# Optimization experiments

Measured on AMD Instinct MI355X. Metric: run time of the kernel, lower is better.

Reference implementation:

```python
import jax, jax.numpy as jnp
import numpy as np

K = 5            # kernel_size per dim
KD = K ** 3      # 125 spline weight slots
DIM = 3
NUM_GRAPHS = 64
# (n_nodes, n_edges, c_in, c_mid, c_out) per pyramid level
LEVELS = [(20000, 320000, 1, 32, 64), (10000, 160000, 1, 64, 64),
          (5000, 80000, 1, 64, 64), (2500, 40000, 1, 64, 64), (1250, 20000, 1, 64, 64)]


def setup_inputs() -> dict:
    key = jax.random.key(0)
    inp = {}
    for i, (n, e, cin, c1, c2) in enumerate(LEVELS, start=1):
        ks = jax.random.split(jax.random.fold_in(key, i), 8)
        inp[f'x{i}'] = jax.random.normal(ks[0], (n, cin), jnp.float32)
        inp[f'pseudo{i}'] = jax.random.uniform(ks[1], (e, DIM), jnp.float32)  # in [0,1)
        inp[f'edge_index{i}'] = jax.random.randint(ks[2], (2, e), 0, n)
        inp[f'batch{i}'] = jnp.sort(jax.random.randint(ks[3], (n,), 0, NUM_GRAPHS))
        inp[f'W{i}a'] = 0.1 * jax.random.normal(ks[4], (KD, cin, c1), jnp.float32)
        inp[f'root{i}a'] = 0.1 * jax.random.normal(ks[5], (cin, c1), jnp.float32)
        inp[f'bias{i}a'] = jnp.zeros((c1,), jnp.float32)
        inp[f'W{i}b'] = 0.1 * jax.random.normal(ks[6], (KD, c1, c2), jnp.float32)
        inp[f'root{i}b'] = 0.1 * jax.random.normal(ks[7], (c1, c2), jnp.float32)
        inp[f'bias{i}b'] = jnp.zeros((c2,), jnp.float32)
    kf = jax.random.fold_in(key, 99)
    inp['fc_w'] = 0.05 * jax.random.normal(kf, (5 * 64, 10), jnp.float32)
    inp['fc_b'] = jnp.zeros((10,), jnp.float32)
    return inp


def _spline_conv(x, src, dst, pseudo, W, Wroot, bias):
    """Degree-1 open B-spline conv (torch_spline_conv), mean aggregation + root weight."""
    n, cin = x.shape
    v = pseudo * (K - 1)                       # [E,3], pseudo in [0,1)
    k0 = jnp.floor(v).astype(jnp.int32)        # lower knot index per dim
    frac = v - k0                              # fractional part per dim
    xs = x[src]                                # [E,cin] gather source feats
    # accumulate basis-weighted source features per (target node, kernel slot)
    acc = jnp.zeros((n, KD, cin), x.dtype)
    for bits in range(2 ** DIM):               # 8 corner combinations of linear spline
        w = jnp.ones((src.shape[0],), x.dtype)
        idx = jnp.zeros((src.shape[0],), jnp.int32)
        for d in range(DIM):
            b = (bits >> d) & 1
            w = w * (frac[:, d] if b else 1.0 - frac[:, d])
            idx = idx * K + (k0[:, d] + b)
        acc = acc.at[dst, idx].add(w[:, None] * xs)
    deg = jnp.zeros((n,), x.dtype).at[dst].add(1.0)
    out = jnp.einsum('nki,kio->no', acc, W) / jnp.maximum(deg, 1.0)[:, None]
    return out + x @ Wroot + bias


def _readout(f, batch):
    s = jax.ops.segment_sum(f, batch, num_segments=NUM_GRAPHS)
    cnt = jax.ops.segment_sum(jnp.ones((f.shape[0],), f.dtype), batch, num_segments=NUM_GRAPHS)
    return s / jnp.maximum(cnt, 1.0)[:, None]   # scatter_mean


def _level(x, ei, ps, bt, Wa, ra, ba, Wb, rb, bb):
    f = jax.nn.relu(_spline_conv(x, ei[0], ei[1], ps, Wa, ra, ba))
    f = jax.nn.relu(_spline_conv(f, ei[0], ei[1], ps, Wb, rb, bb))
    return _readout(f, bt)


def reference(x1, pseudo1, edge_index1, batch1, W1a, root1a, bias1a, W1b, root1b, bias1b,
              x2, pseudo2, edge_index2, batch2, W2a, root2a, bias2a, W2b, root2b, bias2b,
              x3, pseudo3, edge_index3, batch3, W3a, root3a, bias3a, W3b, root3b, bias3b,
              x4, pseudo4, edge_index4, batch4, W4a, root4a, bias4a, W4b, root4b, bias4b,
              x5, pseudo5, edge_index5, batch5, W5a, root5a, bias5a, W5b, root5b, bias5b,
              fc_w, fc_b):
    levels = [
        (x1, edge_index1, pseudo1, batch1, W1a, root1a, bias1a, W1b, root1b, bias1b),
        (x2, edge_index2, pseudo2, batch2, W2a, root2a, bias2a, W2b, root2b, bias2b),
        (x3, edge_index3, pseudo3, batch3, W3a, root3a, bias3a, W3b, root3b, bias3b),
        (x4, edge_index4, pseudo4, batch4, W4a, root4a, bias4a, W4b, root4b, bias4b),
        (x5, edge_index5, pseudo5, batch5, W5a, root5a, bias5a, W5b, root5b, bias5b),
    ]
    res = [_level(*lv) for lv in levels]
    h = jnp.concatenate(res, axis=1)            # [B,320]; eval mode -> dropout is identity
    logits = h @ fc_w + fc_b                    # [B,10]
    return jax.nn.log_softmax(logits, axis=1)
```

## Files before the change

### kernel.cpp

```cpp
#include <hip/hip_runtime.h>
#include <hip/hip_fp16.h>
#include <math.h>

#define NUM_GRAPHS 64

typedef unsigned short ushortT;
typedef __attribute__((ext_vector_type(8))) short bf16x8;
typedef __attribute__((ext_vector_type(4))) float f32x4;

constexpr int cN[5]       = {20000, 10000, 5000, 2500, 1250};
constexpr int cE[5]       = {320000, 160000, 80000, 40000, 20000};
constexpr int cNOFF[6]    = {0, 20000, 30000, 35000, 37500, 38750};
constexpr int cEOFF[6]    = {0, 320000, 480000, 560000, 600000, 620000};
constexpr int cEBLKOFF[6] = {0, 1250, 1875, 2188, 2345, 2424};
constexpr int cNBLKOFF[6] = {0, 79, 119, 139, 149, 154};
constexpr int cMT[5]      = {5064, 2564, 1314, 689, 377};
constexpr int cTILEOFF[6] = {0, 5064, 7628, 8942, 9631, 10008};
constexpr int cSEOFF[6]   = {0, 324096, 488192, 572288, 616384, 640512};
constexpr int cF1OFF[6]   = {0, 640000, 1280000, 1600000, 1760000, 1840000};
constexpr int cWOFF[6]    = {0, 32000, 96000, 160000, 224000, 288000};
constexpr int cABLK[6]    = {0, 1250, 1875, 2188, 2345, 2424};
constexpr int cRBOFF[5]   = {0, 256, 768, 1280, 1792};
constexpr int cWAOFF[6]   = {0, 512, 1536, 2560, 3584, 4608};
constexpr int cRGB[6]     = {0, 313, 470, 549, 589, 609};
constexpr int cPAIR[6]    = {0, 2532, 3814, 4471, 4816, 5005};

struct P5f { const float* p[5]; };
struct P5i { const int* p[5]; };

__device__ __forceinline__ int lvl_e(int b) {
    return (b >= cEBLKOFF[4]) ? 4 : (b >= cEBLKOFF[3]) ? 3 : (b >= cEBLKOFF[2]) ? 2 : (b >= cEBLKOFF[1]) ? 1 : 0;
}
__device__ __forceinline__ int lvl_n(int b) {
    return (b >= cNBLKOFF[4]) ? 4 : (b >= cNBLKOFF[3]) ? 3 : (b >= cNBLKOFF[2]) ? 2 : (b >= cNBLKOFF[1]) ? 1 : 0;
}

__device__ __forceinline__ ushortT f2bf(float f) {
    union { float f; unsigned int u; } v; v.f = f;
    unsigned int r = (v.u + 0x7FFFu + ((v.u >> 16) & 1u)) >> 16;
    return (ushortT)r;
}
__device__ __forceinline__ float h2f_lo(unsigned int u) {
    return __half2float(__ushort_as_half((ushortT)(u & 0xFFFFu)));
}
__device__ __forceinline__ float h2f_hi(unsigned int u) {
    return __half2float(__ushort_as_half((ushortT)(u >> 16)));
}

__global__ void k_hist(P5f PS, P5i EI, int* __restrict__ dcnt, int* __restrict__ bb) {
    int b = blockIdx.x;
    int l = lvl_e(b);
    int lb = b - cEBLKOFF[l];
    int E = cE[l];
    __shared__ int h[64];
    int t = threadIdx.x;
    if (t < 64) h[t] = 0;
    __syncthreads();
    int e = lb * 256 + t;
    if (e < E) {
        atomicAdd(&dcnt[cNOFF[l] + EI.p[l][E + e]], 1);
        const float* ps = PS.p[l];
        int c = (int)floorf(ps[e * 3] * 4.f) * 16 + (int)floorf(ps[e * 3 + 1] * 4.f) * 4
              + (int)floorf(ps[e * 3 + 2] * 4.f);
        atomicAdd(&h[c], 1);
    }
    __syncthreads();
    if (t < 64) bb[(size_t)b * 64 + t] = h[t];
}

__global__ void k_cellscan(int* __restrict__ bb_all, int* __restrict__ csPad,
                           int* __restrict__ cellTot, int* __restrict__ cot_all) {
    int l = blockIdx.x;
    int c = threadIdx.x;
    int* bb = bb_all + (size_t)cEBLKOFF[l] * 64;
    int nblk = cEBLKOFF[l + 1] - cEBLKOFF[l];
    int run = 0;
    int b = 0;
    for (; b + 16 <= nblk; b += 16) {
        int v[16];
#pragma unroll
        for (int u = 0; u < 16; u++) v[u] = bb[(b + u) * 64 + c];
#pragma unroll
        for (int u = 0; u < 16; u++) { bb[(b + u) * 64 + c] = run; run += v[u]; }
    }
    for (; b < nblk; b++) { int v = bb[b * 64 + c]; bb[b * 64 + c] = run; run += v; }
    int tot = run;
    cellTot[l * 64 + c] = tot;
    int tiles = (tot + 63) >> 6;
    int x = tiles;
#pragma unroll
    for (int off = 1; off < 64; off <<= 1) { int y = __shfl_up(x, off, 64); if (c >= off) x += y; }
    int tileBase = x - tiles;
    csPad[l * 64 + c] = tileBase * 64;
    int* cot = cot_all + cTILEOFF[l];
    for (int i = 0; i < tiles; i++) {
        int vv = tot - (i << 6); if (vv > 64) vv = 64;
        cot[tileBase + i] = c | (vv << 8);
    }
    int nT = __shfl(x, 63, 64);
    int mt = cMT[l];
    for (int i = nT + c; i < mt; i += 64) cot[i] = -1;
}

__global__ void k_nscan1(const int* __restrict__ dcnt, int* __restrict__ dbase, int* __restrict__ bsum) {
    int b = blockIdx.x;
    int l = lvl_n(b);
    int lb = b - cNBLKOFF[l];
    int n = cN[l];
    __shared__ int sh[256];
    int t = threadIdx.x;
    int i = lb * 256 + t;
    int v = (i < n) ? dcnt[cNOFF[l] + i] : 0;
    sh[t] = v;
    __syncthreads();
    for (int off = 1; off < 256; off <<= 1) {
        int y = (t >= off) ? sh[t - off] : 0;
        __syncthreads();
        sh[t] += y;
        __syncthreads();
    }
    if (i < n) dbase[cNOFF[l] + i] = sh[t] - v;
    if (t == 255) bsum[b] = sh[255];
}

__global__ void k_nscan2(const int* __restrict__ bsum, int* __restrict__ boff) {
    int l = blockIdx.x;
    int o = cNBLKOFF[l];
    int nb = cNBLKOFF[l + 1] - o;
    int t = threadIdx.x;
    int v = (t < nb) ? bsum[o + t] : 0;
    int s = v;
#pragma unroll
    for (int off = 1; off < 64; off <<= 1) { int y = __shfl_up(s, off, 64); if (t >= off) s += y; }
    int tot = __shfl(s, 63, 64);
    if (t < nb) boff[o + t] = s - v;
    int t2 = t + 64;
    int v2 = (t2 < nb) ? bsum[o + t2] : 0;
    int s2 = v2;
#pragma unroll
    for (int off = 1; off < 64; off <<= 1) { int y = __shfl_up(s2, off, 64); if (t >= off) s2 += y; }
    if (t2 < nb) boff[o + t2] = tot + s2 - v2;
}

__global__ void k_scatter(P5f PS, P5i EI, const int* __restrict__ bb, const int* __restrict__ csPad,
                          const int* __restrict__ dbase, const int* __restrict__ boff,
                          int* __restrict__ rank,
                          int4* __restrict__ cbrec, int4* __restrict__ darec,
                          int* __restrict__ cpos) {
    int b = blockIdx.x;
    int l = lvl_e(b);
    int lb = b - cEBLKOFF[l];
    int E = cE[l];
    __shared__ int base[64];
    __shared__ int cnt[64];
    int t = threadIdx.x;
    if (t < 64) { base[t] = bb[(size_t)b * 64 + t] + csPad[l * 64 + t]; cnt[t] = 0; }
    __syncthreads();
    int e = lb * 256 + t;
    if (e >= E) return;
    const float* ps = PS.p[l];
    float v0 = ps[e * 3] * 4.f, v1 = ps[e * 3 + 1] * 4.f, v2 = ps[e * 3 + 2] * 4.f;
    float f0 = floorf(v0), f1v = floorf(v1), f2v = floorf(v2);
    int c = (int)f0 * 16 + (int)f1v * 4 + (int)f2v;
    int r = atomicAdd(&cnt[c], 1);
    int posc = base[c] + r;
    const int* ei = EI.p[l];
    int src = ei[e];
    int dst = ei[E + e];
    int posd = dbase[cNOFF[l] + dst] + boff[cNBLKOFF[l] + (dst >> 8)]
             + atomicAdd(&rank[cNOFF[l] + dst], 1);
    unsigned int fxfy = (unsigned int)__half_as_ushort(__float2half(v0 - f0))
                      | ((unsigned int)__half_as_ushort(__float2half(v1 - f1v)) << 16);
    unsigned int fzp  = (unsigned int)__half_as_ushort(__float2half(v2 - f2v));
    int4 rc;
    rc.x = src; rc.y = 0; rc.z = (int)fxfy; rc.w = (int)fzp;
    cbrec[cSEOFF[l] + posc] = rc;
    int4 rd;
    rd.x = src | (dst << 16); rd.y = c; rd.z = (int)fxfy; rd.w = (int)fzp;
    darec[cEOFF[l] + posd] = rd;
    cpos[cEOFF[l] + posd] = posc;
}

__global__ void k_wswz(P5f WB, P5f RootB, P5f WA,
                       uint4* __restrict__ hi4, uint4* __restrict__ rb, uint4* __restrict__ wa) {
    int idx = blockIdx.x * 256 + threadIdx.x;
    if (idx >= 294912) return;
    if (idx < 288000) {
        int l = (idx >= 224000) ? 4 : (idx >= 160000) ? 3 : (idx >= 96000) ? 2 : (idx >= 32000) ? 1 : 0;
        int local = idx - cWOFF[l];
        int T = l ? 2 : 1, C = l ? 64 : 32;
        int lane = local & 63;
        int blk = (local >> 6) & 3;
        int rest = local >> 8;
        int st = rest % T, s = rest / T;
        int q = lane >> 4, n = blk * 16 + (lane & 15);
        const float* W = WB.p[l];
        union { ushortT u[8]; uint4 v; } ph;
#pragma unroll
        for (int j = 0; j < 8; j++) {
            int k = st * 32 + q * 8 + j;
            ph.u[j] = f2bf(W[((size_t)s * C + k) * 64 + n]);
        }
        hi4[idx] = ph.v;
    } else if (idx < 290304) {
        int id2 = idx - 288000;
        int l = (id2 >= 1792) ? 4 : (id2 >= 1280) ? 3 : (id2 >= 768) ? 2 : (id2 >= 256) ? 1 : 0;
        int local = id2 - cRBOFF[l];
        int lane = local & 63;
        int w = (local >> 6) & 3;
        int st = local >> 8;
        int q = lane >> 4, n = w * 16 + (lane & 15);
        const float* R = RootB.p[l];
        union { ushortT u[8]; uint4 v; } ph;
#pragma unroll
        for (int j = 0; j < 8; j++) {
            int k = st * 32 + q * 8 + j;
            ph.u[j] = f2bf(R[k * 64 + n]);
        }
        rb[id2] = ph.v;
    } else {
        int id3 = idx - 290304;
        int l = (id3 >= cWAOFF[4]) ? 4 : (id3 >= cWAOFF[3]) ? 3 : (id3 >= cWAOFF[2]) ? 2 : (id3 >= cWAOFF[1]) ? 1 : 0;
        int local = id3 - cWAOFF[l];
        int C1 = l ? 64 : 32;
        int numN = C1 / 16;
        int lane = local & 63;
        int rest = local >> 6;
        int nb = rest % numN, st = rest / numN;
        int q = lane >> 4, n = nb * 16 + (lane & 15);
        const float* Wsrc = WA.p[l];
        union { ushortT u[8]; uint4 v; } ph;
#pragma unroll
        for (int j = 0; j < 8; j++) {
            int k = st * 32 + q * 8 + j;
            ph.u[j] = (k < 125) ? f2bf(Wsrc[k * C1 + n]) : (ushortT)0;
        }
        wa[id3] = ph.v;
    }
}

__launch_bounds__(256)
__global__ void conv_a_fused(P5f X, P5f RootA, P5f BiasA,
                             const int4* __restrict__ darec, const uint4* __restrict__ wasw,
                             const int* __restrict__ dbase, const int* __restrict__ boff,
                             const int* __restrict__ dcnt, ushortT* __restrict__ f1bf) {
    __shared__ float S[16 * 126];
    __shared__ ushortT Sbf[16 * 136];
    __shared__ int infoS[256];
    __shared__ unsigned int fxyS[256];
    __shared__ unsigned int fzS[256];
    __shared__ float xsS[256];
    int b = blockIdx.x;
    int l = (b >= cABLK[4]) ? 4 : (b >= cABLK[3]) ? 3 : (b >= cABLK[2]) ? 2 : (b >= cABLK[1]) ? 1 : 0;
    int node0 = (b - cABLK[l]) * 16;
    int n = cN[l];
    int nn = n - node0; if (nn > 16) nn = 16;
    int t = threadIdx.x;
    for (int i = t; i < 16 * 126; i += 256) S[i] = 0.f;
    const int* db = dbase + cNOFF[l];
    const int* bo = boff + cNBLKOFF[l];
    int estart = db[node0] + bo[node0 >> 8];
    int vend = node0 + nn;
    int eend = (vend >= n) ? cE[l] : (db[vend] + bo[vend >> 8]);
    const float* x = X.p[l];
    const int4* dr = darec + cEOFF[l];
    const int bx = t & 1, by = (t >> 1) & 1, bz = (t >> 2) & 1;
    for (int cs = estart; cs < eend; cs += 256) {
        int p = cs + t;
        if (p < eend) {
            int4 r = dr[p];
            infoS[t] = ((((unsigned int)r.x) >> 16) - node0) * 64 + r.y;
            fxyS[t] = (unsigned int)r.z;
            fzS[t] = (unsigned int)r.w;
            xsS[t] = x[r.x & 0xFFFF];
        }
        __syncthreads();
        int ne = eend - cs; if (ne > 256) ne = 256;
        for (int j = (t >> 3); j < ne; j += 32) {
            int info = infoS[j];
            int nl = info >> 6, cell = info & 63;
            unsigned int uz = fxyS[j];
            float fx = h2f_lo(uz), fy = h2f_hi(uz), fz = h2f_lo(fzS[j]);
            float xs = xsS[j];
            int cx = cell >> 4, cy = (cell >> 2) & 3, cz = cell & 3;
            int slot = (cx + bx) * 25 + (cy + by) * 5 + (cz + bz);
            float wc = (bx ? fx : 1.f - fx) * (by ? fy : 1.f - fy) * (bz ? fz : 1.f - fz);
            atomicAdd(&S[nl * 126 + slot], wc * xs);
        }
        __syncthreads();
    }
    for (int i = t; i < 16 * 128; i += 256) {
        int node = i >> 7, k = i & 127;
        float v = (k < 126) ? S[node * 126 + k] : 0.f;
        Sbf[node * 136 + k] = f2bf(v);
    }
    __syncthreads();
    int lane = t & 63, w = t >> 6;
    int C1 = l ? 64 : 32;
    int numN = C1 >> 4;
    if (w < numN) {
        int q = lane >> 4, m = lane & 15;
        const uint4* wl = wasw + cWAOFF[l];
        f32x4 acc = (f32x4){0.f, 0.f, 0.f, 0.f};
#pragma unroll
        for (int st = 0; st < 4; st++) {
            bf16x8 a = *(const bf16x8*)&Sbf[m * 136 + st * 32 + q * 8];
            bf16x8 bw = __builtin_bit_cast(bf16x8, wl[(st * numN + w) * 64 + lane]);
            acc = __builtin_amdgcn_mfma_f32_16x16x32_bf16(a, bw, acc, 0, 0, 0);
        }
        int ch = w * 16 + m;
        float rv = RootA.p[l][ch], bv = BiasA.p[l][ch];
        const int* dcl = dcnt + cNOFF[l];
        ushortT* f1bfl = f1bf + cF1OFF[l];
#pragma unroll
        for (int rr = 0; rr < 4; rr++) {
            int row = q * 4 + rr;
            if (row < nn) {
                int gnode = node0 + row;
                int dv = dcl[gnode];
                float d = (float)(dv > 1 ? dv : 1);
                float o = acc[rr] / d + x[gnode] * rv + bv;
                f1bfl[(size_t)gnode * C1 + ch] = f2bf(fmaxf(o, 0.f));
            }
        }
    }
}

__launch_bounds__(256)
__global__ void k_rgemm(const ushortT* __restrict__ f1bf, const uint4* __restrict__ rb,
                        float* __restrict__ f2) {
    int b = blockIdx.x;
    int l = (b >= cRGB[4]) ? 4 : (b >= cRGB[3]) ? 3 : (b >= cRGB[2]) ? 2 : (b >= cRGB[1]) ? 1 : 0;
    int node0 = (b - cRGB[l]) * 64;
    int n = cN[l];
    int nn = n - node0; if (nn > 64) nn = 64;
    int t = threadIdx.x;
    int lane = t & 63, w = t >> 6;
    int q = lane >> 4, m = lane & 15;
    const int CIN = l ? 64 : 32;
    const int T = l ? 2 : 1;
    const ushortT* fl = f1bf + cF1OFF[l];
    const uint4* rbl = rb + cRBOFF[l];
    f32x4 C[4];
#pragma unroll
    for (int mt = 0; mt < 4; mt++) C[mt] = (f32x4){0.f, 0.f, 0.f, 0.f};
    for (int st = 0; st < T; st++) {
        bf16x8 bh = __builtin_bit_cast(bf16x8, rbl[(st * 4 + w) * 64 + lane]);
#pragma unroll
        for (int mt = 0; mt < 4; mt++) {
            int row = 16 * mt + m;
            int nr = node0 + row; if (nr > n - 1) nr = n - 1;
            bf16x8 a = *(const bf16x8*)&fl[(size_t)nr * CIN + st * 32 + q * 8];
            C[mt] = __builtin_amdgcn_mfma_f32_16x16x32_bf16(a, bh, C[mt], 0, 0, 0);
        }
    }
#pragma unroll
    for (int mt = 0; mt < 4; mt++)
#pragma unroll
        for (int rr = 0; rr < 4; rr++) {
            int row = 16 * mt + q * 4 + rr;
            if (row < nn)
                f2[(size_t)(cNOFF[l] + node0 + row) * 64 + 16 * w + m] = C[mt][rr];
        }
}

template<int CIN>
__device__ __forceinline__ void conv_b_tile_compute(
    const uint4* __restrict__ whiL, __half* __restrict__ pout,
    bf16x8 (&ahr)[4][CIN / 32], const float* __restrict__ wxy,
    const float* __restrict__ fzp, int cell, int tb, int lane, int wv) {
    const int T = CIN / 32;
    int q = lane >> 4, m = lane & 15;
    int cx = cell >> 4, cy = (cell >> 2) & 3, cz = cell & 3;
    float fzr[16];
#pragma unroll
    for (int mt = 0; mt < 4; mt++)
#pragma unroll
        for (int rr = 0; rr < 4; rr++)
            fzr[mt * 4 + rr] = fzp[16 * mt + q * 4 + rr];

    uint4 wb[2][2 * T];
    auto loadw = [&](int xy, uint4* dst) {
        int bx = xy & 1, by = xy >> 1;
        int s0 = (cx + bx) * 25 + (cy + by) * 5 + cz;
#pragma unroll
        for (int st = 0; st < T; st++) {
            dst[st]     = whiL[((size_t)(s0 * T + st) * 4 + wv) * 64 + lane];
            dst[T + st] = whiL[((size_t)((s0 + 1) * T + st) * 4 + wv) * 64 + lane];
        }
    };
    loadw(0, wb[0]);

    f32x4 acc[4];
#pragma unroll
    for (int mt = 0; mt < 4; mt++) acc[mt] = (f32x4){0.f, 0.f, 0.f, 0.f};

#pragma unroll
    for (int xy = 0; xy < 4; xy++) {
        uint4* cur = wb[xy & 1];
        if (xy < 3) loadw(xy + 1, wb[(xy + 1) & 1]);
        f32x4 C0[4], C1[4];
#pragma unroll
        for (int mt = 0; mt < 4; mt++) {
            C0[mt] = (f32x4){0.f, 0.f, 0.f, 0.f};
            C1[mt] = (f32x4){0.f, 0.f, 0.f, 0.f};
        }
#pragma unroll
        for (int st = 0; st < T; st++) {
            bf16x8 b0 = __builtin_bit_cast(bf16x8, cur[st]);
            bf16x8 b1 = __builtin_bit_cast(bf16x8, cur[T + st]);
#pragma unroll
            for (int mt = 0; mt < 4; mt++) {
                C0[mt] = __builtin_amdgcn_mfma_f32_16x16x32_bf16(ahr[mt][st], b0, C0[mt], 0, 0, 0);
                C1[mt] = __builtin_amdgcn_mfma_f32_16x16x32_bf16(ahr[mt][st], b1, C1[mt], 0, 0, 0);
            }
        }
        const float* wrow = &wxy[xy * 64];
#pragma unroll
        for (int mt = 0; mt < 4; mt++)
#pragma unroll
            for (int rr = 0; rr < 4; rr++) {
                float wxyv = wrow[16 * mt + q * 4 + rr];
                float dlt = C1[mt][rr] - C0[mt][rr];
                float tt = fmaf(fzr[mt * 4 + rr], dlt, C0[mt][rr]);
                acc[mt][rr] = fmaf(wxyv, tt, acc[mt][rr]);
            }
    }
#pragma unroll
    for (int mt = 0; mt < 4; mt++)
#pragma unroll
        for (int rr = 0; rr < 4; rr++) {
            int row = 16 * mt + q * 4 + rr;
            pout[(size_t)(tb + row) * 64 + 16 * wv + m] = __float2half(acc[mt][rr]);
        }
}

template<int CIN>
__device__ __forceinline__ void conv_b_pair(
    const ushortT* __restrict__ f1bfl, const int4* __restrict__ cbl,
    const uint4* __restrict__ whiL, __half* __restrict__ pout,
    int d0, int d1, int tb0, int tb1, int lane, int wv,
    float* __restrict__ wxy0, float* __restrict__ fz0,
    float* __restrict__ wxy1, float* __restrict__ fz1) {
    const int T = CIN / 32;
    int q = lane >> 4, m = lane & 15;
    bool has1 = d1 >= 0;
    int cell0 = d0 & 63, v0 = d0 >> 8;
    int cell1 = has1 ? (d1 & 63) : 0, v1 = has1 ? (d1 >> 8) : 0;

    int4 r0, r1;
    if (lane < v0) r0 = cbl[tb0 + lane]; else { r0.x = 0; r0.y = 0; r0.z = 0; r0.w = 0; }
    if (lane < v1) r1 = cbl[tb1 + lane]; else { r1.x = 0; r1.y = 0; r1.z = 0; r1.w = 0; }

    {
        unsigned int uz = (unsigned int)r0.z;
        float fx = h2f_lo(uz), fy = h2f_hi(uz);
        float gx = 1.f - fx, gy = 1.f - fy;
        wxy0[0 * 64 + lane] = gx * gy;
        wxy0[1 * 64 + lane] = fx * gy;
        wxy0[2 * 64 + lane] = gx * fy;
        wxy0[3 * 64 + lane] = fx * fy;
        fz0[lane] = h2f_lo((unsigned int)r0.w);
    }
    {
        unsigned int uz = (unsigned int)r1.z;
        float fx = h2f_lo(uz), fy = h2f_hi(uz);
        float gx = 1.f - fx, gy = 1.f - fy;
        wxy1[0 * 64 + lane] = gx * gy;
        wxy1[1 * 64 + lane] = fx * gy;
        wxy1[2 * 64 + lane] = gx * fy;
        wxy1[3 * 64 + lane] = fx * fy;
        fz1[lane] = h2f_lo((unsigned int)r1.w);
    }
    __builtin_amdgcn_wave_barrier();

    bf16x8 ahr0[4][T], ahr1[4][T];
#pragma unroll
    for (int mt = 0; mt < 4; mt++) {
        int src = __shfl(r0.x, 16 * mt + m, 64);
#pragma unroll
        for (int st = 0; st < T; st++)
            ahr0[mt][st] = *(const bf16x8*)&f1bfl[(size_t)src * CIN + st * 32 + q * 8];
    }
    if (has1) {
#pragma unroll
        for (int mt = 0; mt < 4; mt++) {
            int src = __shfl(r1.x, 16 * mt + m, 64);
#pragma unroll
            for (int st = 0; st < T; st++)
                ahr1[mt][st] = *(const bf16x8*)&f1bfl[(size_t)src * CIN + st * 32 + q * 8];
        }
    }

    conv_b_tile_compute<CIN>(whiL, pout, ahr0, wxy0, fz0, cell0, tb0, lane, wv);
    if (has1)
        conv_b_tile_compute<CIN>(whiL, pout, ahr1, wxy1, fz1, cell1, tb1, lane, wv);
}

__launch_bounds__(256, 3)
__global__ void conv_b_all(const ushortT* __restrict__ f1bf, const int4* __restrict__ cbrec,
                           const uint4* __restrict__ whi, const int* __restrict__ cot,
                           __half* __restrict__ Ph) {
    __shared__ float wxyS[4][2][256];
    __shared__ float fzS[4][2][64];
    int t = threadIdx.x;
    int wv = t >> 6, lane = t & 63;
    int b = blockIdx.x;
    int l = (b >= cPAIR[4]) ? 4 : (b >= cPAIR[3]) ? 3 : (b >= cPAIR[2]) ? 2 : (b >= cPAIR[1]) ? 1 : 0;
    int p = b - cPAIR[l];
    int t0 = 2 * p, t1 = t0 + 1;
    const int* cotl = cot + cTILEOFF[l];
    int d0 = cotl[t0];
    int d1 = (t1 < cMT[l]) ? cotl[t1] : -1;
    if (d0 < 0) return;
    int tb0 = t0 * 64, tb1 = t1 * 64;
    if (l == 0)
        conv_b_pair<32>(f1bf, cbrec, whi, Ph, d0, d1, tb0, tb1, lane, wv,
                        wxyS[wv][0], fzS[wv][0], wxyS[wv][1], fzS[wv][1]);
    else
        conv_b_pair<64>(f1bf + cF1OFF[l], cbrec + cSEOFF[l], whi + cWOFF[l],
                        Ph + (size_t)cSEOFF[l] * 64, d0, d1, tb0, tb1, lane, wv,
                        wxyS[wv][0], fzS[wv][0], wxyS[wv][1], fzS[wv][1]);
}

__launch_bounds__(256)
__global__ void node_b_all(const __half* __restrict__ Ph, const int* __restrict__ cpos,
                           const int* __restrict__ dbase, const int* __restrict__ boff,
                           const int* __restrict__ dcnt, P5f BiasB, float* __restrict__ f2) {
    int lane = threadIdx.x & 63;
    int blk = blockIdx.x;
    int l, node;
    if (blk < 5000) {
        l = 0;
        node = blk * 4 + (threadIdx.x >> 6);
        if (node >= 20000) return;
    } else {
        const int NB2[4] = {0, 2500, 3750, 4375};
        int b2 = blk - 5000;
        int li = (b2 >= 4375) ? 3 : (b2 >= 3750) ? 2 : (b2 >= 2500) ? 1 : 0;
        l = li + 1;
        node = (b2 - NB2[li]) * 4 + (threadIdx.x >> 6);
        if (node >= cN[l]) return;
    }
    int start = dbase[cNOFF[l] + node] + boff[cNBLKOFF[l] + (node >> 8)];
    int deg = dcnt[cNOFF[l] + node];
    const __half* PhL = Ph + (size_t)cSEOFF[l] * 64;
    const int* cposL = cpos + cEOFF[l];
    float* f2row = f2 + (size_t)(cNOFF[l] + node) * 64;
    float s0 = 0.f, s1 = 0.f, s2 = 0.f, s3 = 0.f;
    int k = 0;
    for (; k + 4 <= deg; k += 4) {
        int r0 = cposL[start + k];
        int r1 = cposL[start + k + 1];
        int r2 = cposL[start + k + 2];
        int r3 = cposL[start + k + 3];
        s0 += __half2float(PhL[(size_t)r0 * 64 + lane]);
        s1 += __half2float(PhL[(size_t)r1 * 64 + lane]);
        s2 += __half2float(PhL[(size_t)r2 * 64 + lane]);
        s3 += __half2float(PhL[(size_t)r3 * 64 + lane]);
    }
    for (; k < deg; k++) s0 += __half2float(PhL[(size_t)cposL[start + k] * 64 + lane]);
    float s = (s0 + s1) + (s2 + s3);
    s /= (float)(deg > 1 ? deg : 1);
    s += f2row[lane] + BiasB.p[l][lane];
    f2row[lane] = fmaxf(s, 0.f);
}

__launch_bounds__(256)
__global__ void k_read(const float* __restrict__ f2, P5i Batch,
                       float* __restrict__ hsum, float* __restrict__ gcnt) {
    const int RC[5] = {0, 1250, 1875, 2188, 2345};
    int t = threadIdx.x;
    int lane = t & 63;
    int w = blockIdx.x * 4 + (t >> 6);
    if (w >= 2424) return;
    int l = (w >= 2345) ? 4 : (w >= 2188) ? 3 : (w >= 1875) ? 2 : (w >= 1250) ? 1 : 0;
    int base = (w - RC[l]) * 16;
    int Nl = cN[l];
    int nn = Nl - base; if (nn > 16) nn = 16;
    const int* batch = Batch.p[l];
    const float* fb = f2 + (size_t)(cNOFF[l] + base) * 64;
    int curg = -1; float hacc = 0.f; int crun = 0;
    for (int j = 0; j < nn; j++) {
        int g = batch[base + j];
        if (g != curg) {
            if (curg >= 0) {
                atomicAdd(&hsum[curg * 320 + l * 64 + lane], hacc);
                if (lane == 0) atomicAdd(&gcnt[l * 64 + curg], (float)crun);
            }
            curg = g; hacc = 0.f; crun = 0;
        }
        hacc += fb[(size_t)j * 64 + lane];
        crun++;
    }
    if (curg >= 0) {
        atomicAdd(&hsum[curg * 320 + l * 64 + lane], hacc);
        if (lane == 0) atomicAdd(&gcnt[l * 64 + curg], (float)crun);
    }
}

__global__ void fc_kernel(const float* __restrict__ hsum, const float* __restrict__ gcnt,
                          const float* __restrict__ fcw, const float* __restrict__ fcb,
                          float* __restrict__ out) {
    int g = blockIdx.x;
    int lane = threadIdx.x;
    float partial[10];
#pragma unroll
    for (int t = 0; t < 10; t++) partial[t] = 0.f;
#pragma unroll
    for (int k = 0; k < 5; k++) {
        int j = k * 64 + lane;
        float c = fmaxf(gcnt[k * 64 + g], 1.f);
        float h = hsum[g * 320 + j] / c;
        const float* fw = fcw + j * 10;
#pragma unroll
        for (int t = 0; t < 10; t++) partial[t] = fmaf(h, fw[t], partial[t]);
    }
#pragma unroll
    for (int off = 32; off >= 1; off >>= 1)
#pragma unroll
        for (int t = 0; t < 10; t++) partial[t] += __shfl_xor(partial[t], off, 64);
    if (lane == 0) {
        float logit[10];
#pragma unroll
        for (int t = 0; t < 10; t++) logit[t] = partial[t] + fcb[t];
        float m = logit[0];
#pragma unroll
        for (int t = 1; t < 10; t++) m = fmaxf(m, logit[t]);
        float sum = 0.f;
#pragma unroll
        for (int t = 0; t < 10; t++) sum += expf(logit[t] - m);
        float lse = m + logf(sum);
#pragma unroll
        for (int t = 0; t < 10; t++) out[g * 10 + t] = logit[t] - lse;
    }
}

extern "C" void kernel_launch(void* const* d_in, const int* in_sizes, int n_in,
                              void* d_out, int out_size, void* d_ws, size_t ws_size,
                              hipStream_t stream) {
    int* wsI = (int*)d_ws;
    int*   dcnt  = wsI;
    int*   rank  = dcnt + 38750;
    float* hsum  = (float*)(rank + 38750);
    float* gcnt  = hsum + 20480;
    float* f2    = gcnt + 320;
    int*   dbase = (int*)(f2 + 2480000);
    int*   bsum  = dbase + 38750;
    int*   boff  = bsum + 160;
    int*   cpos  = boff + 160;
    int*   bb    = cpos + 620000;
    int*   csPad = bb + 155136;
    int*   cellTot = csPad + 320;
    int*   cot   = cellTot + 320;
    int4*  cbrec = (int4*)(((size_t)(cot + 10008) + 15) & ~(size_t)15);
    int4*  darec = cbrec + 640512;
    ushortT* f1bf = (ushortT*)(darec + 620000);
    uint4* whi   = (uint4*)(((size_t)(f1bf + 1840000) + 15) & ~(size_t)15);
    uint4* rbsw  = whi + 288000;
    uint4* wasw  = rbsw + 2304;
    __half* Ph   = (__half*)(wasw + 4608);

    hipMemsetAsync(dcnt, 0, (size_t)(38750 * 2 + 20480 + 320) * sizeof(int), stream);

    P5f PS, X, WA, RootA, BiasA, WB, RootB, BiasB;
    P5i EI, Batch;
    for (int l = 0; l < 5; l++) {
        const int b = l * 10;
        X.p[l]     = (const float*)d_in[b + 0];
        PS.p[l]    = (const float*)d_in[b + 1];
        EI.p[l]    = (const int*)d_in[b + 2];
        Batch.p[l] = (const int*)d_in[b + 3];
        WA.p[l]    = (const float*)d_in[b + 4];
        RootA.p[l] = (const float*)d_in[b + 5];
        BiasA.p[l] = (const float*)d_in[b + 6];
        WB.p[l]    = (const float*)d_in[b + 7];
        RootB.p[l] = (const float*)d_in[b + 8];
        BiasB.p[l] = (const float*)d_in[b + 9];
    }

    k_hist<<<2424, 256, 0, stream>>>(PS, EI, dcnt, bb);
    k_cellscan<<<5, 64, 0, stream>>>(bb, csPad, cellTot, cot);
    k_nscan1<<<154, 256, 0, stream>>>(dcnt, dbase, bsum);
    k_nscan2<<<5, 64, 0, stream>>>(bsum, boff);
    k_scatter<<<2424, 256, 0, stream>>>(PS, EI, bb, csPad, dbase, boff, rank,
                                        cbrec, darec, cpos);
    k_wswz<<<1152, 256, 0, stream>>>(WB, RootB, WA, whi, rbsw, wasw);

    conv_a_fused<<<2424, 256, 0, stream>>>(X, RootA, BiasA, darec, wasw,
                                           dbase, boff, dcnt, f1bf);

    k_rgemm<<<609, 256, 0, stream>>>(f1bf, rbsw, f2);

    conv_b_all<<<5005, 256, 0, stream>>>(f1bf, cbrec, whi, cot, Ph);
    node_b_all<<<9688, 256, 0, stream>>>(Ph, cpos, dbase, boff, dcnt, BiasB, f2);

    k_read<<<606, 256, 0, stream>>>(f2, Batch, hsum, gcnt);
    fc_kernel<<<64, 64, 0, stream>>>(hsum, gcnt, (const float*)d_in[50], (const float*)d_in[51],
                                     (float*)d_out);
}
```

Measured before the change: 467.9 us.

## Stage gathered source rows into LDS via async global_load_lds with swizzle

In conv_b_pair, the gathered source-feature rows are no longer loaded straight into registers. Each wave issues async global-to-LDS copies into a swizzled shared buffer for both tiles of the pair, waits with partial vmcnt only for the first tile, and computes it while the second tile's loads are still in flight. This is meant to overlap gather latency with MFMA compute and to cut register pressure from holding two sets of A fragments. In exchange, LDS use rises and launch bounds drop from 3 to 2 blocks per CU. All four waves still issue the same loads into a shared region, so the gather work across waves is still duplicated.

```diff
diff --git a/kernel.cpp b/kernel.cpp
--- a/kernel.cpp
+++ b/kernel.cpp
@@ -365,6 +365,41 @@
 }
 
 template<int CIN>
+__device__ __forceinline__ void stage_issue(const ushortT* __restrict__ f1bfl, int srcx,
+                                            ushortT* lregion, int lane) {
+    const int NC = CIN / 8;
+#pragma unroll
+    for (int i = 0; i < NC; i++) {
+        int s = i * 64 + lane;
+        int row = s / NC;
+        int cp = s & (NC - 1);
+        int chunk = cp ^ (row & (NC - 1));
+        int src = __shfl(srcx, row, 64);
+        const ushortT* gp = f1bfl + (size_t)src * CIN + chunk * 8;
+        __builtin_amdgcn_global_load_lds(
+            (const __attribute__((address_space(1))) void*)gp,
+            (__attribute__((address_space(3))) void*)(lregion + (size_t)i * 512),
+            16, 0, 0);
+    }
+}
+
+template<int CIN>
+__device__ __forceinline__ void read_ahr(const ushortT* st, bf16x8 (&ahr)[4][CIN / 32],
+                                         int q, int m) {
+    const int NC = CIN / 8;
+#pragma unroll
+    for (int mt = 0; mt < 4; mt++) {
+        int row = 16 * mt + m;
+#pragma unroll
+        for (int s = 0; s < CIN / 32; s++) {
+            int chunk = s * 4 + q;
+            int cp = chunk ^ (row & (NC - 1));
+            ahr[mt][s] = *(const bf16x8*)&st[(size_t)row * NC * 8 + cp * 8];
+        }
+    }
+}
+
+template<int CIN>
 __device__ __forceinline__ void conv_b_tile_compute(
     const uint4* __restrict__ whiL, __half* __restrict__ pout,
     bf16x8 (&ahr)[4][CIN / 32], const float* __restrict__ wxy,
@@ -440,9 +475,11 @@
     const ushortT* __restrict__ f1bfl, const int4* __restrict__ cbl,
     const uint4* __restrict__ whiL, __half* __restrict__ pout,
     int d0, int d1, int tb0, int tb1, int lane, int wv,
+    ushortT* stage0, ushortT* stage1,
     float* __restrict__ wxy0, float* __restrict__ fz0,
     float* __restrict__ wxy1, float* __restrict__ fz1) {
     const int T = CIN / 32;
+    const int NC = CIN / 8;
     int q = lane >> 4, m = lane & 15;
     bool has1 = d1 >= 0;
     int cell0 = d0 & 63, v0 = d0 >> 8;
@@ -474,35 +511,35 @@
     }
     __builtin_amdgcn_wave_barrier();
 
-    bf16x8 ahr0[4][T], ahr1[4][T];
-#pragma unroll
-    for (int mt = 0; mt < 4; mt++) {
-        int src = __shfl(r0.x, 16 * mt + m, 64);
-#pragma unroll
-        for (int st = 0; st < T; st++)
-            ahr0[mt][st] = *(const bf16x8*)&f1bfl[(size_t)src * CIN + st * 32 + q * 8];
-    }
+    stage_issue<CIN>(f1bfl, r0.x, stage0, lane);
+    if (has1) stage_issue<CIN>(f1bfl, r1.x, stage1, lane);
+
     if (has1) {
-#pragma unroll
-        for (int mt = 0; mt < 4; mt++) {
-            int src = __shfl(r1.x, 16 * mt + m, 64);
-#pragma unroll
-            for (int st = 0; st < T; st++)
-                ahr1[mt][st] = *(const bf16x8*)&f1bfl[(size_t)src * CIN + st * 32 + q * 8];
-        }
-    }
-
-    conv_b_tile_compute<CIN>(whiL, pout, ahr0, wxy0, fz0, cell0, tb0, lane, wv);
-    if (has1)
-        conv_b_tile_compute<CIN>(whiL, pout, ahr1, wxy1, fz1, cell1, tb1, lane, wv);
-}
-
-__launch_bounds__(256, 3)
+        if (CIN == 64) asm volatile("s_waitcnt vmcnt(8)" ::: "memory");
+        else           asm volatile("s_waitcnt vmcnt(4)" ::: "memory");
+    } else {
+        asm volatile("s_waitcnt vmcnt(0)" ::: "memory");
+    }
+
+    bf16x8 ahr[4][T];
+    read_ahr<CIN>(stage0, ahr, q, m);
+    conv_b_tile_compute<CIN>(whiL, pout, ahr, wxy0, fz0, cell0, tb0, lane, wv);
+
+    if (has1) {
+        asm volatile("s_waitcnt vmcnt(0)" ::: "memory");
+        read_ahr<CIN>(stage1, ahr, q, m);
+        conv_b_tile_compute<CIN>(whiL, pout, ahr, wxy1, fz1, cell1, tb1, lane, wv);
+    }
+    (void)NC;
+}
+
+__launch_bounds__(256, 2)
 __global__ void conv_b_all(const ushortT* __restrict__ f1bf, const int4* __restrict__ cbrec,
                            const uint4* __restrict__ whi, const int* __restrict__ cot,
                            __half* __restrict__ Ph) {
-    __shared__ float wxyS[4][2][256];
-    __shared__ float fzS[4][2][64];
+    __shared__ __align__(16) ushortT stageS[2][4096];
+    __shared__ float wxyS[2][256];
+    __shared__ float fzS[2][64];
     int t = threadIdx.x;
     int wv = t >> 6, lane = t & 63;
     int b = blockIdx.x;
@@ -516,11 +553,11 @@
     int tb0 = t0 * 64, tb1 = t1 * 64;
     if (l == 0)
         conv_b_pair<32>(f1bf, cbrec, whi, Ph, d0, d1, tb0, tb1, lane, wv,
-                        wxyS[wv][0], fzS[wv][0], wxyS[wv][1], fzS[wv][1]);
+                        stageS[0], stageS[1], wxyS[0], fzS[0], wxyS[1], fzS[1]);
     else
         conv_b_pair<64>(f1bf + cF1OFF[l], cbrec + cSEOFF[l], whi + cWOFF[l],
                         Ph + (size_t)cSEOFF[l] * 64, d0, d1, tb0, tb1, lane, wv,
-                        wxyS[wv][0], fzS[wv][0], wxyS[wv][1], fzS[wv][1]);
+                        stageS[0], stageS[1], wxyS[0], fzS[0], wxyS[1], fzS[1]);
 }
 
 __launch_bounds__(256)
```

After: 432.1 us. -7.6%, faster.
